# Performance work log

Measured on AMD Instinct MI355X. Metric: run time of the kernel, lower is better.

Reference implementation:

```python
import jax, jax.numpy as jnp
import numpy as np

NUM_BITS_ACTS = 8
NUM_BITS_PARAMS = 8
NUM_BITS_ACCUM = 32


def quantized_range(num_bits):
    # distiller-style signed range: [-2^(n-1), 2^(n-1)-1]
    n = 2.0 ** num_bits
    return -n / 2.0, n / 2.0 - 1.0


def sym_scale(num_bits, sat_abs):
    # scale = (2^(n-1)-1) / max_abs
    return (2.0 ** (num_bits - 1) - 1.0) / sat_abs


def quant_clamp(t, scale, qmin, qmax):
    return jnp.clip(jnp.round(t * scale), qmin, qmax)


def setup_inputs() -> dict:
    key = jax.random.key(0)
    kx, kw = jax.random.split(key)
    x = jax.random.normal(kx, (8192, 4096), dtype=jnp.float32)
    W = jax.random.normal(kw, (4096, 4096), dtype=jnp.float32)  # [out, in]
    return {"x": x, "W": W}


def reference(x, W):
    acts_min, acts_max = quantized_range(NUM_BITS_ACTS)
    params_min, params_max = quantized_range(NUM_BITS_PARAMS)
    accum_min, accum_max = quantized_range(NUM_BITS_ACCUM)

    # __init__: quantize weights once (symmetric, max-abs)
    w_scale = sym_scale(NUM_BITS_PARAMS, jnp.max(jnp.abs(W)))
    W_q = quant_clamp(W, w_scale, params_min, params_max)

    # pre_quantized_forward: input scale from max-abs, quantize-clamp input
    in_scale = sym_scale(NUM_BITS_ACTS, jnp.max(jnp.abs(x)))
    x_q = quant_clamp(x, in_scale, acts_min, acts_max)

    # wrapped Linear in integer domain, clamp to accumulator range
    accum = jnp.clip(x_q @ W_q.T, accum_min, accum_max)  # [8192, 4096]

    # post_quantized_forward: requantize accumulator to output range
    accum_scale = in_scale * w_scale
    accum_max_abs = jnp.max(jnp.abs(accum))
    y_f_max_abs = accum_max_abs / accum_scale
    out_scale = sym_scale(NUM_BITS_ACTS, y_f_max_abs)
    requant_scale = out_scale / accum_scale

    out_q = quant_clamp(accum, requant_scale, acts_min, acts_max)
    out_f = out_q / out_scale  # dequantize
    return out_f
```

## Files before the change

### kernel.cpp

```cpp
#include <hip/hip_runtime.h>
#include <stdint.h>


using i32x4 = __attribute__((ext_vector_type(4))) int;

#define M_DIM 8192
#define N_DIM 4096
#define K_DIM 4096

#define BM 256
#define BN 256
#define BKB 128
#define NKT (K_DIM / BKB)

__global__ void k_init(unsigned* sc) {
    sc[0] = 0u;
    sc[1] = 0u;
    sc[2] = 0u;
}

__global__ __launch_bounds__(256) void k_absmax2(const float4* __restrict__ x,
                                                 const float4* __restrict__ w,
                                                 unsigned* __restrict__ sc) {
    const bool isX = blockIdx.x < 2048;
    const float4* src = isX ? x : w;
    const int n4 = isX ? (M_DIM * K_DIM / 4) : (N_DIM * K_DIM / 4);
    const int brel = isX ? blockIdx.x : (blockIdx.x - 2048);
    const int nb = isX ? 2048 : 1024;
    unsigned m = 0;
    for (int i = brel * 256 + threadIdx.x; i < n4; i += nb * 256) {
        float4 v = src[i];
        unsigned a = __float_as_uint(v.x) & 0x7fffffffu;
        unsigned b = __float_as_uint(v.y) & 0x7fffffffu;
        unsigned c = __float_as_uint(v.z) & 0x7fffffffu;
        unsigned d = __float_as_uint(v.w) & 0x7fffffffu;
        m = max(m, max(max(a, b), max(c, d)));
    }
    for (int off = 32; off; off >>= 1)
        m = max(m, (unsigned)__shfl_xor((int)m, off));
    __shared__ unsigned wm[4];
    int ln = threadIdx.x & 63, wv = threadIdx.x >> 6;
    if (ln == 0) wm[wv] = m;
    __syncthreads();
    if (threadIdx.x == 0)
        atomicMax(sc + (isX ? 0 : 1), max(max(wm[0], wm[1]), max(wm[2], wm[3])));
}

__global__ __launch_bounds__(256) void k_quant2(const float4* __restrict__ x,
                                                const float4* __restrict__ w,
                                                unsigned* __restrict__ xq,
                                                unsigned* __restrict__ wq,
                                                const unsigned* __restrict__ sc) {
    const bool isX = blockIdx.x < 2048;
    const float4* src = isX ? x : w;
    unsigned* dst = isX ? xq : wq;
    const int n4 = isX ? (M_DIM * K_DIM / 4) : (N_DIM * K_DIM / 4);
    const int brel = isX ? blockIdx.x : (blockIdx.x - 2048);
    const int nb = isX ? 2048 : 1024;
    const float scale = 127.0f / __uint_as_float(sc[isX ? 0 : 1]);
    for (int i = brel * 256 + threadIdx.x; i < n4; i += nb * 256) {
        float4 v = src[i];
        int q0 = min(127, max(-128, (int)rintf(v.x * scale)));
        int q1 = min(127, max(-128, (int)rintf(v.y * scale)));
        int q2 = min(127, max(-128, (int)rintf(v.z * scale)));
        int q3 = min(127, max(-128, (int)rintf(v.w * scale)));
        dst[i] = (unsigned)(q0 & 0xff) | ((unsigned)(q1 & 0xff) << 8) |
                 ((unsigned)(q2 & 0xff) << 16) | ((unsigned)(q3 & 0xff) << 24);
    }
}

__global__ __launch_bounds__(512, 2) void k_gemm(const char* __restrict__ Aq,
                                                 const char* __restrict__ Bq,
                                                 int* __restrict__ C,
                                                 unsigned* __restrict__ maxAcc) {
    __shared__ __align__(16) char lds[131072];
    __shared__ int wmax[8];

    const int t = threadIdx.x;
    const int ln = t & 63;
    const int wv = t >> 6;
    const int wr = wv >> 2;
    const int wc = wv & 3;
    const int lr = ln & 15;
    const int lk = ln >> 4;

    const int bid = blockIdx.x;
    const int swz = (bid & 7) * 64 + (bid >> 3);
    const int bx = swz & 15;
    const int by = swz >> 4;
    const int arow0 = by * BM;
    const int brow0 = bx * BN;

    const int cs0 = lk ^ (lr & 7);
    const int aoff0 = (((wr << 7) + lr) << 7) + (cs0 << 4);
    const int aoff1 = aoff0 ^ 64;
    const int boff0 = (((wc << 6) + lr) << 7) + (cs0 << 4);
    const int boff1 = boff0 ^ 64;

    int voffA[2], voffB[2];
#pragma unroll
    for (int it = 0; it < 2; ++it) {
        const int chunk = it * 512 + (wv << 6) + ln;
        const int row = chunk >> 3;
        const int gc = (chunk & 7) ^ (row & 7);
        voffA[it] = (arow0 + row) * 4096 + (gc << 4);
        voffB[it] = (brow0 + row) * 4096 + (gc << 4);
    }

    i32x4 acc[8][4];
#pragma unroll
    for (int i = 0; i < 8; ++i)
#pragma unroll
        for (int j = 0; j < 4; ++j) acc[i][j] = (i32x4)(0);

    auto STAGE = [&](int kt, int j) {
        const int slot = kt & 1;
        const int koff = kt * 128 + (j & 1) * 524288;
        const bool isA = (j < 2);
        const char* gbase = isA ? Aq : Bq;
        const int* voff = isA ? voffA : voffB;
        char* lbase = lds + (isA ? 0 : 65536) + (slot << 15) + ((j & 1) << 14) + (wv << 10);
#pragma unroll
        for (int it = 0; it < 2; ++it) {
            const char* g = gbase + (unsigned)(voff[it] + koff);
            __builtin_amdgcn_global_load_lds(
                (const __attribute__((address_space(1))) void*)g,
                (__attribute__((address_space(3))) void*)(lbase + (it << 13)), 16, 0, 0);
        }
    };

    STAGE(0, 0); STAGE(0, 1); STAGE(0, 2); STAGE(0, 3);
    STAGE(1, 2); STAGE(1, 3);
    asm volatile("s_waitcnt vmcnt(4)" ::: "memory");
    __builtin_amdgcn_s_barrier();
    __builtin_amdgcn_sched_barrier(0);

    for (int kt = 0; kt < NKT; ++kt) {
        const int sl = (kt & 1) << 15;
        const char* pA0 = lds + sl + aoff0;
        const char* pA1 = lds + sl + aoff1;
        const char* pB0 = lds + 65536 + sl + boff0;
        const char* pB1 = lds + 65536 + sl + boff1;
        i32x4 a[4][2], b[4][2];

#pragma unroll
        for (int mi = 0; mi < 4; ++mi) {
            a[mi][0] = *(const i32x4*)(pA0 + (mi << 11));
            a[mi][1] = *(const i32x4*)(pA1 + (mi << 11));
        }
#pragma unroll
        for (int ni = 0; ni < 4; ++ni) {
            b[ni][0] = *(const i32x4*)(pB0 + (ni << 11));
            b[ni][1] = *(const i32x4*)(pB1 + (ni << 11));
        }
        if (kt + 1 < NKT) { STAGE(kt + 1, 0); STAGE(kt + 1, 1); }
        __builtin_amdgcn_s_setprio(1);
#pragma unroll
        for (int kh = 0; kh < 2; ++kh)
#pragma unroll
            for (int mi = 0; mi < 4; ++mi)
#pragma unroll
                for (int ni = 0; ni < 4; ++ni)
                    acc[mi][ni] = __builtin_amdgcn_mfma_i32_16x16x64_i8(
                        a[mi][kh], b[ni][kh], acc[mi][ni], 0, 0, 0);
        __builtin_amdgcn_s_setprio(0);
#pragma unroll
        for (int mi = 0; mi < 4; ++mi) {
            a[mi][0] = *(const i32x4*)(pA0 + ((mi + 4) << 11));
            a[mi][1] = *(const i32x4*)(pA1 + ((mi + 4) << 11));
        }
        __builtin_amdgcn_s_barrier();
        __builtin_amdgcn_sched_barrier(0);

        if (kt + 2 < NKT) {
            STAGE(kt + 2, 2); STAGE(kt + 2, 3);
            asm volatile("s_waitcnt vmcnt(4)" ::: "memory");
        } else {
            asm volatile("s_waitcnt vmcnt(0)" ::: "memory");
        }
        __builtin_amdgcn_s_setprio(1);
#pragma unroll
        for (int kh = 0; kh < 2; ++kh)
#pragma unroll
            for (int mi = 0; mi < 4; ++mi)
#pragma unroll
                for (int ni = 0; ni < 4; ++ni)
                    acc[mi + 4][ni] = __builtin_amdgcn_mfma_i32_16x16x64_i8(
                        a[mi][kh], b[ni][kh], acc[mi + 4][ni], 0, 0, 0);
        __builtin_amdgcn_s_setprio(0);
        __builtin_amdgcn_s_barrier();
        __builtin_amdgcn_sched_barrier(0);
    }

    int amax = 0;
#pragma unroll
    for (int mi = 0; mi < 8; ++mi) {
#pragma unroll
        for (int ni = 0; ni < 4; ++ni) {
            const int row0 = arow0 + (wr << 7) + (mi << 4) + (lk << 2);
            const int col  = brow0 + (wc << 6) + (ni << 4) + lr;
            i32x4 v = acc[mi][ni];
#pragma unroll
            for (int j = 0; j < 4; ++j) {
                C[(size_t)(row0 + j) * N_DIM + col] = v[j];
                int a = v[j] < 0 ? -v[j] : v[j];
                amax = max(amax, a);
            }
        }
    }
    for (int off = 32; off; off >>= 1)
        amax = max(amax, __shfl_xor(amax, off));
    if (ln == 0) wmax[wv] = amax;
    __syncthreads();
    if (t == 0) {
        int m = wmax[0];
#pragma unroll
        for (int i = 1; i < 8; ++i) m = max(m, wmax[i]);
        atomicMax(maxAcc, (unsigned)m);
    }
}

__global__ __launch_bounds__(256) void k_requant(int4* __restrict__ buf, int n4,
                                                 const unsigned* __restrict__ sc) {
    const float maxX = __uint_as_float(sc[0]);
    const float maxW = __uint_as_float(sc[1]);
    const float maxA = (float)(int)sc[2];
    const float in_scale = 127.0f / maxX;
    const float w_scale  = 127.0f / maxW;
    const float accum_scale = in_scale * w_scale;
    const float requant = 127.0f / maxA;
    const float out_scale = requant * accum_scale;
    int stride = gridDim.x * blockDim.x;
    for (int i = blockIdx.x * blockDim.x + threadIdx.x; i < n4; i += stride) {
        int4 v = buf[i];
        float4 o;
        o.x = fminf(127.f, fmaxf(-128.f, rintf((float)v.x * requant))) / out_scale;
        o.y = fminf(127.f, fmaxf(-128.f, rintf((float)v.y * requant))) / out_scale;
        o.z = fminf(127.f, fmaxf(-128.f, rintf((float)v.z * requant))) / out_scale;
        o.w = fminf(127.f, fmaxf(-128.f, rintf((float)v.w * requant))) / out_scale;
        ((float4*)buf)[i] = o;
    }
}

extern "C" void kernel_launch(void* const* d_in, const int* in_sizes, int n_in,
                              void* d_out, int out_size, void* d_ws, size_t ws_size,
                              hipStream_t stream) {
    const float* x = (const float*)d_in[0];
    const float* W = (const float*)d_in[1];

    unsigned* sc = (unsigned*)d_ws;
    char* xq = (char*)d_ws + 256;
    char* wq = xq + (size_t)M_DIM * K_DIM;

    k_init<<<1, 1, 0, stream>>>(sc);
    k_absmax2<<<3072, 256, 0, stream>>>((const float4*)x, (const float4*)W, sc);
    k_quant2<<<3072, 256, 0, stream>>>((const float4*)x, (const float4*)W,
                                       (unsigned*)xq, (unsigned*)wq, sc);
    k_gemm<<<(M_DIM / BM) * (N_DIM / BN), 512, 0, stream>>>(xq, wq, (int*)d_out, sc + 2);
    k_requant<<<2048, 256, 0, stream>>>((int4*)d_out, M_DIM * N_DIM / 4, sc);
}
```

Baseline: 282.0 us.

## Halve GEMM K-tile to 64 bytes and raise occupancy to four blocks per CU

Cuts the int8 GEMM K-step from 128 to 64 bytes, which halves LDS use to 64KB and lets launch bounds ask for four 512-thread blocks per CU instead of two. To match, it rewrites the LDS swizzle for 64-byte rows, the global-to-LDS staging (one load per stage), the wait counts and the fragment loads. The aim is more resident waves to hide latency. The cost is twice as many barriers and iterations per tile and tighter register limits, with 128 accumulator registers per lane, which may cause spills.

```diff
diff --git a/kernel.cpp b/kernel.cpp
--- a/kernel.cpp
+++ b/kernel.cpp
@@ -10,7 +10,7 @@
 
 #define BM 256
 #define BN 256
-#define BKB 128
+#define BKB 64
 #define NKT (K_DIM / BKB)
 
 __global__ void k_init(unsigned* sc) {
@@ -69,11 +69,11 @@
     }
 }
 
-__global__ __launch_bounds__(512, 2) void k_gemm(const char* __restrict__ Aq,
+__global__ __launch_bounds__(512, 4) void k_gemm(const char* __restrict__ Aq,
                                                  const char* __restrict__ Bq,
                                                  int* __restrict__ C,
                                                  unsigned* __restrict__ maxAcc) {
-    __shared__ __align__(16) char lds[131072];
+    __shared__ __align__(16) char lds[65536];
     __shared__ int wmax[8];
 
     const int t = threadIdx.x;
@@ -91,21 +91,18 @@
     const int arow0 = by * BM;
     const int brow0 = bx * BN;
 
-    const int cs0 = lk ^ (lr & 7);
-    const int aoff0 = (((wr << 7) + lr) << 7) + (cs0 << 4);
-    const int aoff1 = aoff0 ^ 64;
-    const int boff0 = (((wc << 6) + lr) << 7) + (cs0 << 4);
-    const int boff1 = boff0 ^ 64;
-
-    int voffA[2], voffB[2];
-#pragma unroll
-    for (int it = 0; it < 2; ++it) {
-        const int chunk = it * 512 + (wv << 6) + ln;
-        const int row = chunk >> 3;
-        const int gc = (chunk & 7) ^ (row & 7);
-        voffA[it] = (arow0 + row) * 4096 + (gc << 4);
-        voffB[it] = (brow0 + row) * 4096 + (gc << 4);
-    }
+    const int sig = (lr + (lr >> 2)) & 3;
+    const int cs = lk ^ sig;
+    const int aoff = ((((wr << 7) + lr) << 6) + (cs << 4));
+    const int boff = ((((wc << 6) + lr) << 6) + (cs << 4));
+
+    const int schunk = (wv << 6) + ln;
+    const int srow = schunk >> 2;
+    const int sgc = (schunk & 3) ^ ((srow + (srow >> 2)) & 3);
+    const int vA0 = (arow0 + srow) * 4096 + (sgc << 4);
+    const int vA1 = (arow0 + 128 + srow) * 4096 + (sgc << 4);
+    const int vB0 = (brow0 + srow) * 4096 + (sgc << 4);
+    const int vB1 = (brow0 + 128 + srow) * 4096 + (sgc << 4);
 
     i32x4 acc[8][4];
 #pragma unroll
@@ -115,78 +112,63 @@
 
     auto STAGE = [&](int kt, int j) {
         const int slot = kt & 1;
-        const int koff = kt * 128 + (j & 1) * 524288;
+        const int koff = kt * 64;
         const bool isA = (j < 2);
+        const int voff = isA ? ((j & 1) ? vA1 : vA0) : ((j & 1) ? vB1 : vB0);
         const char* gbase = isA ? Aq : Bq;
-        const int* voff = isA ? voffA : voffB;
-        char* lbase = lds + (isA ? 0 : 65536) + (slot << 15) + ((j & 1) << 14) + (wv << 10);
-#pragma unroll
-        for (int it = 0; it < 2; ++it) {
-            const char* g = gbase + (unsigned)(voff[it] + koff);
-            __builtin_amdgcn_global_load_lds(
-                (const __attribute__((address_space(1))) void*)g,
-                (__attribute__((address_space(3))) void*)(lbase + (it << 13)), 16, 0, 0);
-        }
+        char* lbase = lds + (isA ? 0 : 32768) + (slot << 14) + ((j & 1) << 13) + (wv << 10);
+        const char* g = gbase + (unsigned)(voff + koff);
+        __builtin_amdgcn_global_load_lds(
+            (const __attribute__((address_space(1))) void*)g,
+            (__attribute__((address_space(3))) void*)lbase, 16, 0, 0);
     };
 
     STAGE(0, 0); STAGE(0, 1); STAGE(0, 2); STAGE(0, 3);
     STAGE(1, 2); STAGE(1, 3);
-    asm volatile("s_waitcnt vmcnt(4)" ::: "memory");
+    asm volatile("s_waitcnt vmcnt(2)" ::: "memory");
     __builtin_amdgcn_s_barrier();
     __builtin_amdgcn_sched_barrier(0);
 
     for (int kt = 0; kt < NKT; ++kt) {
-        const int sl = (kt & 1) << 15;
-        const char* pA0 = lds + sl + aoff0;
-        const char* pA1 = lds + sl + aoff1;
-        const char* pB0 = lds + 65536 + sl + boff0;
-        const char* pB1 = lds + 65536 + sl + boff1;
-        i32x4 a[4][2], b[4][2];
-
-#pragma unroll
-        for (int mi = 0; mi < 4; ++mi) {
-            a[mi][0] = *(const i32x4*)(pA0 + (mi << 11));
-            a[mi][1] = *(const i32x4*)(pA1 + (mi << 11));
-        }
-#pragma unroll
-        for (int ni = 0; ni < 4; ++ni) {
-            b[ni][0] = *(const i32x4*)(pB0 + (ni << 11));
-            b[ni][1] = *(const i32x4*)(pB1 + (ni << 11));
-        }
+        const int sl = (kt & 1) << 14;
+        const char* pA = lds + sl + aoff;
+        const char* pB = lds + 32768 + sl + boff;
+        i32x4 a[4], b[4];
+
+#pragma unroll
+        for (int mi = 0; mi < 4; ++mi)
+            a[mi] = *(const i32x4*)(pA + (mi << 10));
+#pragma unroll
+        for (int ni = 0; ni < 4; ++ni)
+            b[ni] = *(const i32x4*)(pB + (ni << 10));
         if (kt + 1 < NKT) { STAGE(kt + 1, 0); STAGE(kt + 1, 1); }
         __builtin_amdgcn_s_setprio(1);
 #pragma unroll
-        for (int kh = 0; kh < 2; ++kh)
-#pragma unroll
-            for (int mi = 0; mi < 4; ++mi)
-#pragma unroll
-                for (int ni = 0; ni < 4; ++ni)
-                    acc[mi][ni] = __builtin_amdgcn_mfma_i32_16x16x64_i8(
-                        a[mi][kh], b[ni][kh], acc[mi][ni], 0, 0, 0);
+        for (int mi = 0; mi < 4; ++mi)
+#pragma unroll
+            for (int ni = 0; ni < 4; ++ni)
+                acc[mi][ni] = __builtin_amdgcn_mfma_i32_16x16x64_i8(
+                    a[mi], b[ni], acc[mi][ni], 0, 0, 0);
         __builtin_amdgcn_s_setprio(0);
-#pragma unroll
-        for (int mi = 0; mi < 4; ++mi) {
-            a[mi][0] = *(const i32x4*)(pA0 + ((mi + 4) << 11));
-            a[mi][1] = *(const i32x4*)(pA1 + ((mi + 4) << 11));
-        }
         __builtin_amdgcn_s_barrier();
         __builtin_amdgcn_sched_barrier(0);
 
+#pragma unroll
+        for (int mi = 0; mi < 4; ++mi)
+            a[mi] = *(const i32x4*)(pA + ((mi + 4) << 10));
         if (kt + 2 < NKT) {
             STAGE(kt + 2, 2); STAGE(kt + 2, 3);
-            asm volatile("s_waitcnt vmcnt(4)" ::: "memory");
+            asm volatile("s_waitcnt vmcnt(2)" ::: "memory");
         } else {
             asm volatile("s_waitcnt vmcnt(0)" ::: "memory");
         }
         __builtin_amdgcn_s_setprio(1);
 #pragma unroll
-        for (int kh = 0; kh < 2; ++kh)
-#pragma unroll
-            for (int mi = 0; mi < 4; ++mi)
-#pragma unroll
-                for (int ni = 0; ni < 4; ++ni)
-                    acc[mi + 4][ni] = __builtin_amdgcn_mfma_i32_16x16x64_i8(
-                        a[mi][kh], b[ni][kh], acc[mi + 4][ni], 0, 0, 0);
+        for (int mi = 0; mi < 4; ++mi)
+#pragma unroll
+            for (int ni = 0; ni < 4; ++ni)
+                acc[mi + 4][ni] = __builtin_amdgcn_mfma_i32_16x16x64_i8(
+                    a[mi], b[ni], acc[mi + 4][ni], 0, 0, 0);
         __builtin_amdgcn_s_setprio(0);
         __builtin_amdgcn_s_barrier();
         __builtin_amdgcn_sched_barrier(0);
```

Result: slower. 1.099 ms (+289.8%).
